# Performance work log

Measured on AMD Instinct MI355X. Metric: run time of the kernel, lower is better.

Reference implementation:

```python
import jax, jax.numpy as jnp
import numpy as np

DT = 0.1
N_STEPS = 20
STEP_SIZE = DT / N_STEPS


def setup_inputs() -> dict:
    key = jax.random.key(0)
    ks = jax.random.split(key, 8)
    sizes = [1024, 2048, 2048, 10]
    batch = 4096
    inp = {
        "x": jax.random.uniform(ks[0], (batch, sizes[0]), dtype=jnp.float32),
        "w0": jax.random.normal(ks[1], (sizes[0], sizes[1]), dtype=jnp.float32) / np.sqrt(sizes[0]),
        "w1": jax.random.normal(ks[2], (sizes[1], sizes[2]), dtype=jnp.float32) / np.sqrt(sizes[1]),
        "w2": jax.random.normal(ks[3], (sizes[2], sizes[3]), dtype=jnp.float32) / np.sqrt(sizes[2]),
        "b0": jnp.zeros((sizes[1],), jnp.float32),
        "b1": jnp.zeros((sizes[2],), jnp.float32),
        "b2": jnp.zeros((sizes[3],), jnp.float32),
        "s1": jax.random.uniform(ks[4], (batch, sizes[1]), dtype=jnp.float32),
        "s2": jax.random.uniform(ks[5], (batch, sizes[2]), dtype=jnp.float32),
        "s3": jax.random.uniform(ks[6], (batch, sizes[3]), dtype=jnp.float32),
    }
    return inp


def reference(x, w0, w1, w2, b0, b1, b2, s1, s2, s3):
    weights = [w0, w1, w2]
    biases = [b0, b1, b2]
    sig = jax.nn.sigmoid

    def dsig(v):
        s = sig(v)
        return s * (1.0 - s)

    def body(states, _):
        st = list(states)  # [s0(=x, clamped), s1, s2, s3]
        # hidden layers (indices 1..len-2), sequential in-place semantics
        for i in range(1, 3):
            pre = sig(st[i - 1]) @ weights[i - 1] + sig(st[i + 1]) @ weights[i].T + biases[i - 1]
            grad = dsig(st[i]) * pre - st[i]
            st[i] = st[i] - STEP_SIZE * grad
        # output layer (no target / beta=0 in eval mode)
        grad = dsig(st[3]) * (sig(st[2]) @ weights[2] + biases[2]) - st[3]
        st[3] = st[3] - STEP_SIZE * grad
        return tuple(st), None

    init = (x, s1, s2, s3)
    final, _ = jax.lax.scan(body, init, None, length=N_STEPS)
    return final[-1]
```

## Files before the change

kernel.cpp:

```cpp
#include <hip/hip_runtime.h>
#include <cstdint>
#include <cstddef>

using u16 = unsigned short;
using u32 = unsigned int;

typedef __bf16 bf16x8 __attribute__((ext_vector_type(8)));
typedef float f32x4 __attribute__((ext_vector_type(4)));
typedef u16 u16x4 __attribute__((ext_vector_type(4)));

#define DEV __device__ __forceinline__

constexpr float SS = 0.1f / 20.0f;

DEV float sigm(float x) { return 1.0f / (1.0f + __expf(-x)); }

DEV u16 f2bf(float f) {
  union { float f; u32 u; } v; v.f = f;
  u32 r = v.u + 0x7FFFu + ((v.u >> 16) & 1u);
  return (u16)(r >> 16);
}
DEV float bf2f(u16 h) {
  union { u32 u; float f; } v; v.u = ((u32)h) << 16;
  return v.f;
}

__global__ void k_prep(const float* __restrict__ in, float* __restrict__ fcopy,
                       float* __restrict__ sigf32, u16* __restrict__ sigb,
                       u16* __restrict__ rawb, int n) {
  int stride = gridDim.x * blockDim.x;
  for (int i = blockIdx.x * blockDim.x + threadIdx.x; i < n; i += stride) {
    float v = in[i];
    if (fcopy) fcopy[i] = v;
    if (rawb) rawb[i] = f2bf(v);
    if (sigf32 || sigb) {
      float s = sigm(v);
      if (sigf32) sigf32[i] = s;
      if (sigb) sigb[i] = f2bf(s);
    }
  }
}

__global__ void k_transpose_bf16(const float* __restrict__ in, u16* __restrict__ out,
                                 int K, int N) {
  __shared__ float tile[32][33];
  int kb = blockIdx.x * 32, nb = blockIdx.y * 32;
  int tx = threadIdx.x & 31, ty = threadIdx.x >> 5;
#pragma unroll
  for (int i = 0; i < 4; ++i)
    tile[ty + 8 * i][tx] = in[(size_t)(kb + ty + 8 * i) * N + nb + tx];
  __syncthreads();
#pragma unroll
  for (int i = 0; i < 4; ++i)
    out[(size_t)(nb + ty + 8 * i) * K + kb + tx] = f2bf(tile[tx][ty + 8 * i]);
}

DEV void tile_base(int b, int& tm, int& tn) {
  int xcd = b & 7, slot = b >> 3;
  tm = ((((xcd >> 1) << 3) | (slot >> 3))) * 128;
  tn = ((((xcd & 1) << 3) | (slot & 7))) * 128;
}

__global__ void k_init_state(const float* __restrict__ src, float* __restrict__ dst_swz) {
  int b = blockIdx.x;
  int tm, tn; tile_base(b, tm, tn);
  int tid = threadIdx.x, lane = tid & 63, wid = tid >> 6;
  int l15 = lane & 15, lhi = lane >> 4;
  int wm = (wid >> 2) * 64, wn = (wid & 3) * 32;
#pragma unroll
  for (int i = 0; i < 4; ++i)
#pragma unroll
    for (int j = 0; j < 2; ++j) {
      int gr = tm + wm + i * 16 + l15;
      int gc0 = tn + wn + j * 16 + 4 * lhi;
      f32x4 v = *(const f32x4*)(src + (size_t)gr * 2048 + gc0);
      *(f32x4*)(dst_swz + (((size_t)b * 8 + i * 2 + j) * 512 + tid) * 4) = v;
    }
}

template <int MODE>
__launch_bounds__(512, 4)
__global__ void k_gemm(const u16* __restrict__ A, const u16* __restrict__ Bt,
                       int M, int N, int K,
                       const u16* __restrict__ addcb, const float* __restrict__ bias,
                       const float* __restrict__ sig3, const float* __restrict__ w2,
                       float* __restrict__ statef, u16* __restrict__ sigb) {
  constexpr int BM = 128, BN = 128, BK = 64;
  __shared__ __align__(16) u16 Als[2][BM * BK];
  __shared__ __align__(16) u16 Bls[2][BN * BK];
  int b = blockIdx.x;
  int tm, tn; tile_base(b, tm, tn);
  int tid = threadIdx.x;
  int lane = tid & 63, wid = tid >> 6;
  int l15 = lane & 15, lhi = lane >> 4;
  int wm = (wid >> 2) * 64, wn = (wid & 3) * 32;

  const u16* Ag = A + (size_t)tm * K;
  const u16* Bg = Bt + (size_t)tn * K;

  f32x4 acc[4][2] = {};

  auto stage = [&](int buf, int k0) {
#pragma unroll
    for (int rd = 0; rd < 2; ++rd) {
      int S = rd * 512 + tid;
      int row = S >> 3;
      int cs = ((S & 7) ^ (row & 7)) * 8;
      __builtin_amdgcn_global_load_lds(
          (const __attribute__((address_space(1))) u32*)(Ag + (size_t)row * K + k0 + cs),
          (__attribute__((address_space(3))) u32*)(&Als[buf][0] + S * 8), 16, 0, 0);
      __builtin_amdgcn_global_load_lds(
          (const __attribute__((address_space(1))) u32*)(Bg + (size_t)row * K + k0 + cs),
          (__attribute__((address_space(3))) u32*)(&Bls[buf][0] + S * 8), 16, 0, 0);
    }
  };

  auto compute = [&](int buf) {
    __builtin_amdgcn_s_setprio(1);
#pragma unroll
    for (int s = 0; s < 2; ++s) {
      bf16x8 af[4], bfr[2];
#pragma unroll
      for (int i = 0; i < 4; ++i) {
        int row = wm + i * 16 + l15;
        af[i] = *(const bf16x8*)(&Als[buf][0] + row * BK + (((s * 4 + lhi) ^ (row & 7)) * 8));
      }
#pragma unroll
      for (int j = 0; j < 2; ++j) {
        int row = wn + j * 16 + l15;
        bfr[j] = *(const bf16x8*)(&Bls[buf][0] + row * BK + (((s * 4 + lhi) ^ (row & 7)) * 8));
      }
#pragma unroll
      for (int i = 0; i < 4; ++i)
#pragma unroll
        for (int j = 0; j < 2; ++j)
          acc[i][j] = __builtin_amdgcn_mfma_f32_16x16x32_bf16(bfr[j], af[i], acc[i][j], 0, 0, 0);
    }
    __builtin_amdgcn_s_setprio(0);
  };

  const int nt = K / BK;
  stage(0, 0);
  stage(1, BK);
  asm volatile("s_waitcnt vmcnt(4)" ::: "memory");
  __builtin_amdgcn_s_barrier();
  asm volatile("" ::: "memory");

  int t = 0;
  for (; t + 3 < nt; t += 2) {
    compute(0);
    asm volatile("" ::: "memory");
    __builtin_amdgcn_s_barrier();
    asm volatile("" ::: "memory");
    stage(0, (t + 2) * BK);
    asm volatile("s_waitcnt vmcnt(4)" ::: "memory");
    __builtin_amdgcn_s_barrier();
    asm volatile("" ::: "memory");

    compute(1);
    asm volatile("" ::: "memory");
    __builtin_amdgcn_s_barrier();
    asm volatile("" ::: "memory");
    stage(1, (t + 3) * BK);
    asm volatile("s_waitcnt vmcnt(4)" ::: "memory");
    __builtin_amdgcn_s_barrier();
    asm volatile("" ::: "memory");
  }
  compute(0);
  asm volatile("s_waitcnt vmcnt(0)" ::: "memory");
  __builtin_amdgcn_s_barrier();
  asm volatile("" ::: "memory");
  compute(1);

  if constexpr (MODE == 0) {
#pragma unroll
    for (int i = 0; i < 4; ++i)
#pragma unroll
      for (int j = 0; j < 2; ++j) {
        int gc0 = tn + wn + j * 16 + 4 * lhi;
        size_t sidx = (((size_t)b * 8 + i * 2 + j) * 512 + tid) * 4;
        u16x4 sb;
#pragma unroll
        for (int rr = 0; rr < 4; ++rr) sb[rr] = f2bf(acc[i][j][rr] + bias[gc0 + rr]);
        *(u16x4*)(sigb + sidx) = sb;
      }
  } else if constexpr (MODE == 1) {
#pragma unroll
    for (int i = 0; i < 4; ++i)
#pragma unroll
      for (int j = 0; j < 2; ++j) {
        int gr = tm + wm + i * 16 + l15;
        int gc0 = tn + wn + j * 16 + 4 * lhi;
        size_t sidx = (((size_t)b * 8 + i * 2 + j) * 512 + tid) * 4;
        u16x4 ab = *(const u16x4*)(addcb + sidx);
        f32x4 old = *(const f32x4*)(statef + sidx);
        f32x4 nv; u16x4 sb;
#pragma unroll
        for (int rr = 0; rr < 4; ++rr) {
          float pre = acc[i][j][rr] + bf2f(ab[rr]);
          float o = old[rr];
          float sg = sigm(o);
          float n = o - SS * (sg * (1.0f - sg) * pre - o);
          nv[rr] = n; sb[rr] = f2bf(sigm(n));
        }
        *(f32x4*)(statef + sidx) = nv;
        *(u16x4*)(sigb + (size_t)gr * N + gc0) = sb;
      }
  } else {
    float s3v[4][10];
#pragma unroll
    for (int i = 0; i < 4; ++i) {
      int gr = tm + wm + i * 16 + l15;
#pragma unroll
      for (int k = 0; k < 10; ++k) s3v[i][k] = sig3[gr * 10 + k];
    }
#pragma unroll
    for (int j = 0; j < 2; ++j) {
      int gc0 = tn + wn + j * 16 + 4 * lhi;
      float wv[4][10]; f32x4 bb;
#pragma unroll
      for (int rr = 0; rr < 4; ++rr) {
        bb[rr] = bias[gc0 + rr];
#pragma unroll
        for (int k = 0; k < 10; ++k) wv[rr][k] = w2[(gc0 + rr) * 10 + k];
      }
#pragma unroll
      for (int i = 0; i < 4; ++i) {
        int gr = tm + wm + i * 16 + l15;
        size_t sidx = (((size_t)b * 8 + i * 2 + j) * 512 + tid) * 4;
        f32x4 old = *(const f32x4*)(statef + sidx);
        f32x4 nv; u16x4 sb;
#pragma unroll
        for (int rr = 0; rr < 4; ++rr) {
          float ex = bb[rr];
#pragma unroll
          for (int k = 0; k < 10; ++k) ex += s3v[i][k] * wv[rr][k];
          float pre = acc[i][j][rr] + ex;
          float o = old[rr];
          float sg = sigm(o);
          float n = o - SS * (sg * (1.0f - sg) * pre - o);
          nv[rr] = n; sb[rr] = f2bf(sigm(n));
        }
        *(f32x4*)(statef + sidx) = nv;
        *(u16x4*)(sigb + (size_t)gr * N + gc0) = sb;
      }
    }
  }
}

__global__ void k_out(const u16* __restrict__ sigs2b, const float* __restrict__ w2,
                      const float* __restrict__ b2, float* __restrict__ s3f,
                      float* __restrict__ sigs3f, float* __restrict__ outOrNull) {
  int tid = threadIdx.x;
  int r = tid >> 4, l16 = tid & 15;
  int row = blockIdx.x * 16 + r;
  float acc[10] = {};
  const u16* arow = sigs2b + (size_t)row * 2048;
  for (int kb = l16; kb < 256; kb += 16) {
    u16x4 v0 = *(const u16x4*)(arow + kb * 8);
    u16x4 v1 = *(const u16x4*)(arow + kb * 8 + 4);
    float a[8];
#pragma unroll
    for (int e = 0; e < 4; ++e) { a[e] = bf2f(v0[e]); a[e + 4] = bf2f(v1[e]); }
    const float* wr = w2 + (size_t)kb * 80;
#pragma unroll
    for (int e = 0; e < 8; ++e)
#pragma unroll
      for (int n = 0; n < 10; ++n) acc[n] += a[e] * wr[e * 10 + n];
  }
#pragma unroll
  for (int m = 1; m < 16; m <<= 1)
#pragma unroll
    for (int n = 0; n < 10; ++n) acc[n] += __shfl_xor(acc[n], m, 64);
  if (l16 < 10) {
    float pre = 0.0f;
#pragma unroll
    for (int n = 0; n < 10; ++n)
      if (l16 == n) pre = acc[n];
    pre += b2[l16];
    size_t idx = (size_t)row * 10 + l16;
    float old = s3f[idx];
    float sg = sigm(old);
    float nv = old - SS * (sg * (1.0f - sg) * pre - old);
    s3f[idx] = nv;
    sigs3f[idx] = sigm(nv);
    if (outOrNull) outOrNull[idx] = nv;
  }
}

extern "C" void kernel_launch(void* const* d_in, const int* in_sizes, int n_in,
                              void* d_out, int out_size, void* d_ws, size_t ws_size,
                              hipStream_t stream) {
  const float* x  = (const float*)d_in[0];
  const float* w0 = (const float*)d_in[1];
  const float* w1 = (const float*)d_in[2];
  const float* w2 = (const float*)d_in[3];
  const float* b0 = (const float*)d_in[4];
  const float* b1 = (const float*)d_in[5];
  const float* b2 = (const float*)d_in[6];
  const float* s1 = (const float*)d_in[7];
  const float* s2 = (const float*)d_in[8];
  const float* s3 = (const float*)d_in[9];
  float* out = (float*)d_out;

  uint8_t* p = (uint8_t*)d_ws;
  auto alloc = [&](size_t bytes) {
    uint8_t* r = p;
    p += (bytes + 255) & ~(size_t)255;
    return r;
  };
  float* s1f    = (float*)alloc(4096ull * 2048 * 4);
  float* s2f    = (float*)alloc(4096ull * 2048 * 4);
  u16*   addcb  = (u16*)alloc(4096ull * 2048 * 2);
  u16*   sigs1b = (u16*)alloc(4096ull * 2048 * 2);
  u16*   sigs2b = (u16*)alloc(4096ull * 2048 * 2);
  u16*   sigxb  = (u16*)alloc(4096ull * 1024 * 2);
  u16*   w1b    = (u16*)alloc(2048ull * 2048 * 2);
  u16*   w1tb   = (u16*)alloc(2048ull * 2048 * 2);
  u16*   w0tb   = (u16*)alloc(2048ull * 1024 * 2);
  float* s3f    = (float*)alloc(4096ull * 10 * 4);
  float* sigs3f = (float*)alloc(4096ull * 10 * 4);
  (void)ws_size; (void)in_sizes; (void)n_in; (void)out_size;

  auto grid = [](int n) { int g = (n + 255) / 256; return g > 2048 ? 2048 : g; };

  k_prep<<<grid(4096 * 1024), 256, 0, stream>>>(x, nullptr, nullptr, sigxb, nullptr, 4096 * 1024);
  k_prep<<<grid(2048 * 2048), 256, 0, stream>>>(w1, nullptr, nullptr, nullptr, w1b, 2048 * 2048);
  k_prep<<<grid(4096 * 2048), 256, 0, stream>>>(s2, nullptr, nullptr, sigs2b, nullptr, 4096 * 2048);
  k_prep<<<grid(40960), 256, 0, stream>>>(s3, s3f, sigs3f, nullptr, nullptr, 40960);
  k_init_state<<<512, 512, 0, stream>>>(s1, s1f);
  k_init_state<<<512, 512, 0, stream>>>(s2, s2f);
  k_transpose_bf16<<<dim3(1024 / 32, 2048 / 32), 256, 0, stream>>>(w0, w0tb, 1024, 2048);
  k_transpose_bf16<<<dim3(2048 / 32, 2048 / 32), 256, 0, stream>>>(w1, w1tb, 2048, 2048);

  k_gemm<0><<<512, 512, 0, stream>>>(sigxb, w0tb, 4096, 2048, 1024,
                                     nullptr, b0, nullptr, nullptr, nullptr, addcb);

  for (int t = 0; t < 20; ++t) {
    k_gemm<1><<<512, 512, 0, stream>>>(sigs2b, w1b, 4096, 2048, 2048,
                                       addcb, nullptr, nullptr, nullptr, s1f, sigs1b);
    k_gemm<2><<<512, 512, 0, stream>>>(sigs1b, w1tb, 4096, 2048, 2048,
                                       nullptr, b1, sigs3f, w2, s2f, sigs2b);
    k_out<<<256, 256, 0, stream>>>(sigs2b, w2, b2, s3f, sigs3f, (t == 19) ? out : nullptr);
  }
}
```

Measured before the change: 2.503 ms.

## Enlarge GEMM tiles to 256x128 with triple-buffered LDS pipeline

Doubles the GEMM block tile height to 256 rows and gives each wave a 64x64 sub-tile, halving the grid to 256 blocks. Shared memory moves to dynamic allocation with three stages instead of two, and the k-loop becomes a rotating single-step prefetch. This aims to raise MFMA work per LDS and global load and to hide memory latency better. The trade-off is one block per CU with more registers per thread and a large LDS footprint.

```diff
diff --git a/kernel.cpp b/kernel.cpp
--- a/kernel.cpp
+++ b/kernel.cpp
@@ -57,8 +57,8 @@
 
 DEV void tile_base(int b, int& tm, int& tn) {
   int xcd = b & 7, slot = b >> 3;
-  tm = ((((xcd >> 1) << 3) | (slot >> 3))) * 128;
-  tn = ((((xcd & 1) << 3) | (slot & 7))) * 128;
+  tm = ((xcd >> 1) * 4 + (slot >> 3)) * 256;
+  tn = ((xcd & 1) * 8 + (slot & 7)) * 128;
 }
 
 __global__ void k_init_state(const float* __restrict__ src, float* __restrict__ dst_swz) {
@@ -66,119 +66,125 @@
   int tm, tn; tile_base(b, tm, tn);
   int tid = threadIdx.x, lane = tid & 63, wid = tid >> 6;
   int l15 = lane & 15, lhi = lane >> 4;
-  int wm = (wid >> 2) * 64, wn = (wid & 3) * 32;
+  int wm = (wid >> 1) * 64, wn = (wid & 1) * 64;
 #pragma unroll
   for (int i = 0; i < 4; ++i)
 #pragma unroll
-    for (int j = 0; j < 2; ++j) {
+    for (int j = 0; j < 4; ++j) {
       int gr = tm + wm + i * 16 + l15;
       int gc0 = tn + wn + j * 16 + 4 * lhi;
       f32x4 v = *(const f32x4*)(src + (size_t)gr * 2048 + gc0);
-      *(f32x4*)(dst_swz + (((size_t)b * 8 + i * 2 + j) * 512 + tid) * 4) = v;
+      *(f32x4*)(dst_swz + (((size_t)b * 16 + i * 4 + j) * 512 + tid) * 4) = v;
     }
 }
 
 template <int MODE>
-__launch_bounds__(512, 4)
+__launch_bounds__(512, 2)
 __global__ void k_gemm(const u16* __restrict__ A, const u16* __restrict__ Bt,
                        int M, int N, int K,
                        const u16* __restrict__ addcb, const float* __restrict__ bias,
                        const float* __restrict__ sig3, const float* __restrict__ w2,
                        float* __restrict__ statef, u16* __restrict__ sigb) {
-  constexpr int BM = 128, BN = 128, BK = 64;
-  __shared__ __align__(16) u16 Als[2][BM * BK];
-  __shared__ __align__(16) u16 Bls[2][BN * BK];
+  constexpr int BK = 64;
+  extern __shared__ __align__(16) u16 lds_dyn[];
+  u16* const AlsBase = lds_dyn;
+  u16* const BlsBase = lds_dyn + 3 * 16384;
+
   int b = blockIdx.x;
   int tm, tn; tile_base(b, tm, tn);
   int tid = threadIdx.x;
   int lane = tid & 63, wid = tid >> 6;
   int l15 = lane & 15, lhi = lane >> 4;
-  int wm = (wid >> 2) * 64, wn = (wid & 3) * 32;
+  int wm = (wid >> 1) * 64, wn = (wid & 1) * 64;
 
   const u16* Ag = A + (size_t)tm * K;
   const u16* Bg = Bt + (size_t)tn * K;
 
-  f32x4 acc[4][2] = {};
-
-  auto stage = [&](int buf, int k0) {
+  f32x4 acc[4][4] = {};
+
+  auto stage = [&](int p, int k0) {
+    u16* Ap = AlsBase + p * 16384;
+    u16* Bp = BlsBase + p * 8192;
+#pragma unroll
+    for (int rd = 0; rd < 4; ++rd) {
+      int S = rd * 512 + tid;
+      int row = S >> 3;
+      int cs = ((S & 7) ^ (row & 7)) * 8;
+      __builtin_amdgcn_global_load_lds(
+          (const __attribute__((address_space(1))) u32*)(Ag + (size_t)row * K + k0 + cs),
+          (__attribute__((address_space(3))) u32*)(Ap + S * 8), 16, 0, 0);
+    }
 #pragma unroll
     for (int rd = 0; rd < 2; ++rd) {
       int S = rd * 512 + tid;
       int row = S >> 3;
       int cs = ((S & 7) ^ (row & 7)) * 8;
       __builtin_amdgcn_global_load_lds(
-          (const __attribute__((address_space(1))) u32*)(Ag + (size_t)row * K + k0 + cs),
-          (__attribute__((address_space(3))) u32*)(&Als[buf][0] + S * 8), 16, 0, 0);
-      __builtin_amdgcn_global_load_lds(
           (const __attribute__((address_space(1))) u32*)(Bg + (size_t)row * K + k0 + cs),
-          (__attribute__((address_space(3))) u32*)(&Bls[buf][0] + S * 8), 16, 0, 0);
+          (__attribute__((address_space(3))) u32*)(Bp + S * 8), 16, 0, 0);
     }
   };
 
-  auto compute = [&](int buf) {
+  auto compute = [&](int p) {
+    const u16* Ap = AlsBase + p * 16384;
+    const u16* Bp = BlsBase + p * 8192;
     __builtin_amdgcn_s_setprio(1);
 #pragma unroll
     for (int s = 0; s < 2; ++s) {
-      bf16x8 af[4], bfr[2];
+      bf16x8 af[4], bfr[4];
 #pragma unroll
       for (int i = 0; i < 4; ++i) {
         int row = wm + i * 16 + l15;
-        af[i] = *(const bf16x8*)(&Als[buf][0] + row * BK + (((s * 4 + lhi) ^ (row & 7)) * 8));
-      }
-#pragma unroll
-      for (int j = 0; j < 2; ++j) {
+        af[i] = *(const bf16x8*)(Ap + row * BK + (((s * 4 + lhi) ^ (row & 7)) * 8));
+      }
+#pragma unroll
+      for (int j = 0; j < 4; ++j) {
         int row = wn + j * 16 + l15;
-        bfr[j] = *(const bf16x8*)(&Bls[buf][0] + row * BK + (((s * 4 + lhi) ^ (row & 7)) * 8));
+        bfr[j] = *(const bf16x8*)(Bp + row * BK + (((s * 4 + lhi) ^ (row & 7)) * 8));
       }
 #pragma unroll
       for (int i = 0; i < 4; ++i)
 #pragma unroll
-        for (int j = 0; j < 2; ++j)
+        for (int j = 0; j < 4; ++j)
           acc[i][j] = __builtin_amdgcn_mfma_f32_16x16x32_bf16(bfr[j], af[i], acc[i][j], 0, 0, 0);
     }
     __builtin_amdgcn_s_setprio(0);
   };
 
   const int nt = K / BK;
-  stage(0, 0);
-  stage(1, BK);
-  asm volatile("s_waitcnt vmcnt(4)" ::: "memory");
-  __builtin_amdgcn_s_barrier();
-  asm volatile("" ::: "memory");
-
-  int t = 0;
-  for (; t + 3 < nt; t += 2) {
-    compute(0);
+  stage(0, 0); stage(1, BK); stage(2, 2 * BK);
+  int p = 0;
+  for (int t = 0; t < nt - 3; ++t) {
+    asm volatile("s_waitcnt vmcnt(12)" ::: "memory");
+    __builtin_amdgcn_s_barrier();
+    asm volatile("" ::: "memory");
+    compute(p);
     asm volatile("" ::: "memory");
     __builtin_amdgcn_s_barrier();
     asm volatile("" ::: "memory");
-    stage(0, (t + 2) * BK);
-    asm volatile("s_waitcnt vmcnt(4)" ::: "memory");
-    __builtin_amdgcn_s_barrier();
-    asm volatile("" ::: "memory");
-
-    compute(1);
-    asm volatile("" ::: "memory");
-    __builtin_amdgcn_s_barrier();
-    asm volatile("" ::: "memory");
-    stage(1, (t + 3) * BK);
-    asm volatile("s_waitcnt vmcnt(4)" ::: "memory");
-    __builtin_amdgcn_s_barrier();
-    asm volatile("" ::: "memory");
-  }
-  compute(0);
+    stage(p, (t + 3) * BK);
+    p = (p == 2) ? 0 : p + 1;
+  }
+  asm volatile("s_waitcnt vmcnt(12)" ::: "memory");
+  __builtin_amdgcn_s_barrier();
+  asm volatile("" ::: "memory");
+  compute(p); p = (p == 2) ? 0 : p + 1;
+  asm volatile("s_waitcnt vmcnt(6)" ::: "memory");
+  __builtin_amdgcn_s_barrier();
+  asm volatile("" ::: "memory");
+  compute(p); p = (p == 2) ? 0 : p + 1;
   asm volatile("s_waitcnt vmcnt(0)" ::: "memory");
   __builtin_amdgcn_s_barrier();
   asm volatile("" ::: "memory");
-  compute(1);
+  compute(p);
 
   if constexpr (MODE == 0) {
 #pragma unroll
     for (int i = 0; i < 4; ++i)
 #pragma unroll
-      for (int j = 0; j < 2; ++j) {
+      for (int j = 0; j < 4; ++j) {
         int gc0 = tn + wn + j * 16 + 4 * lhi;
-        size_t sidx = (((size_t)b * 8 + i * 2 + j) * 512 + tid) * 4;
+        size_t sidx = (((size_t)b * 16 + i * 4 + j) * 512 + tid) * 4;
         u16x4 sb;
 #pragma unroll
         for (int rr = 0; rr < 4; ++rr) sb[rr] = f2bf(acc[i][j][rr] + bias[gc0 + rr]);
@@ -188,10 +194,10 @@
 #pragma unroll
     for (int i = 0; i < 4; ++i)
 #pragma unroll
-      for (int j = 0; j < 2; ++j) {
+      for (int j = 0; j < 4; ++j) {
         int gr = tm + wm + i * 16 + l15;
         int gc0 = tn + wn + j * 16 + 4 * lhi;
-        size_t sidx = (((size_t)b * 8 + i * 2 + j) * 512 + tid) * 4;
+        size_t sidx = (((size_t)b * 16 + i * 4 + j) * 512 + tid) * 4;
         u16x4 ab = *(const u16x4*)(addcb + sidx);
         f32x4 old = *(const f32x4*)(statef + sidx);
         f32x4 nv; u16x4 sb;
@@ -215,7 +221,7 @@
       for (int k = 0; k < 10; ++k) s3v[i][k] = sig3[gr * 10 + k];
     }
 #pragma unroll
-    for (int j = 0; j < 2; ++j) {
+    for (int j = 0; j < 4; ++j) {
       int gc0 = tn + wn + j * 16 + 4 * lhi;
       float wv[4][10]; f32x4 bb;
 #pragma unroll
@@ -227,7 +233,7 @@
 #pragma unroll
       for (int i = 0; i < 4; ++i) {
         int gr = tm + wm + i * 16 + l15;
-        size_t sidx = (((size_t)b * 8 + i * 2 + j) * 512 + tid) * 4;
+        size_t sidx = (((size_t)b * 16 + i * 4 + j) * 512 + tid) * 4;
         f32x4 old = *(const f32x4*)(statef + sidx);
         f32x4 nv; u16x4 sb;
 #pragma unroll
@@ -322,25 +328,33 @@
   float* sigs3f = (float*)alloc(4096ull * 10 * 4);
   (void)ws_size; (void)in_sizes; (void)n_in; (void)out_size;
 
+  constexpr int LDS_BYTES = 3 * (16384 + 8192) * 2;
+  (void)hipFuncSetAttribute((const void*)k_gemm<0>,
+      hipFuncAttributeMaxDynamicSharedMemorySize, LDS_BYTES);
+  (void)hipFuncSetAttribute((const void*)k_gemm<1>,
+      hipFuncAttributeMaxDynamicSharedMemorySize, LDS_BYTES);
+  (void)hipFuncSetAttribute((const void*)k_gemm<2>,
+      hipFuncAttributeMaxDynamicSharedMemorySize, LDS_BYTES);
+
   auto grid = [](int n) { int g = (n + 255) / 256; return g > 2048 ? 2048 : g; };
 
   k_prep<<<grid(4096 * 1024), 256, 0, stream>>>(x, nullptr, nullptr, sigxb, nullptr, 4096 * 1024);
   k_prep<<<grid(2048 * 2048), 256, 0, stream>>>(w1, nullptr, nullptr, nullptr, w1b, 2048 * 2048);
   k_prep<<<grid(4096 * 2048), 256, 0, stream>>>(s2, nullptr, nullptr, sigs2b, nullptr, 4096 * 2048);
   k_prep<<<grid(40960), 256, 0, stream>>>(s3, s3f, sigs3f, nullptr, nullptr, 40960);
-  k_init_state<<<512, 512, 0, stream>>>(s1, s1f);
-  k_init_state<<<512, 512, 0, stream>>>(s2, s2f);
+  k_init_state<<<256, 512, 0, stream>>>(s1, s1f);
+  k_init_state<<<256, 512, 0, stream>>>(s2, s2f);
   k_transpose_bf16<<<dim3(1024 / 32, 2048 / 32), 256, 0, stream>>>(w0, w0tb, 1024, 2048);
   k_transpose_bf16<<<dim3(2048 / 32, 2048 / 32), 256, 0, stream>>>(w1, w1tb, 2048, 2048);
 
-  k_gemm<0><<<512, 512, 0, stream>>>(sigxb, w0tb, 4096, 2048, 1024,
-                                     nullptr, b0, nullptr, nullptr, nullptr, addcb);
+  k_gemm<0><<<256, 512, LDS_BYTES, stream>>>(sigxb, w0tb, 4096, 2048, 1024,
+                                             nullptr, b0, nullptr, nullptr, nullptr, addcb);
 
   for (int t = 0; t < 20; ++t) {
-    k_gemm<1><<<512, 512, 0, stream>>>(sigs2b, w1b, 4096, 2048, 2048,
-                                       addcb, nullptr, nullptr, nullptr, s1f, sigs1b);
-    k_gemm<2><<<512, 512, 0, stream>>>(sigs1b, w1tb, 4096, 2048, 2048,
-                                       nullptr, b1, sigs3f, w2, s2f, sigs2b);
+    k_gemm<1><<<256, 512, LDS_BYTES, stream>>>(sigs2b, w1b, 4096, 2048, 2048,
+                                               addcb, nullptr, nullptr, nullptr, s1f, sigs1b);
+    k_gemm<2><<<256, 512, LDS_BYTES, stream>>>(sigs1b, w1tb, 4096, 2048, 2048,
+                                               nullptr, b1, sigs3f, w2, s2f, sigs2b);
     k_out<<<256, 256, 0, stream>>>(sigs2b, w2, b2, s3f, sigs3f, (t == 19) ? out : nullptr);
   }
 }
```

New measurement: 2.493 ms. About the same (-0.4%).

## Switch GEMM mainloop to 4-stage BK=32 LDS pipeline with deeper prefetch

Applied to the files above, without the earlier changes.

The GEMM mainloop moves from a double-buffered BK=64 scheme to a four-buffer ring with BK=32 and three K-slices in flight. Each thread issues one global-to-LDS load per operand per stage, and the XOR swizzle is adjusted to 4 chunks per row. The aim is to hide global memory latency better by keeping more loads outstanding. In exchange, each K-step does half as many MFMAs between two barriers, so synchronisation overhead per FLOP doubles, and swizzling over 4 chunks may cause more LDS bank conflicts.

```diff
diff --git a/kernel.cpp b/kernel.cpp
--- a/kernel.cpp
+++ b/kernel.cpp
@@ -85,9 +85,10 @@
                        const u16* __restrict__ addcb, const float* __restrict__ bias,
                        const float* __restrict__ sig3, const float* __restrict__ w2,
                        float* __restrict__ statef, u16* __restrict__ sigb) {
-  constexpr int BM = 128, BN = 128, BK = 64;
-  __shared__ __align__(16) u16 Als[2][BM * BK];
-  __shared__ __align__(16) u16 Bls[2][BN * BK];
+  constexpr int BK = 32;
+  constexpr int BUFE = 128 * BK;
+  __shared__ __align__(16) u16 Als[4][BUFE];
+  __shared__ __align__(16) u16 Bls[4][BUFE];
   int b = blockIdx.x;
   int tm, tn; tile_base(b, tm, tn);
   int tid = threadIdx.x;
@@ -100,77 +101,62 @@
 
   f32x4 acc[4][2] = {};
 
-  auto stage = [&](int buf, int k0) {
-#pragma unroll
-    for (int rd = 0; rd < 2; ++rd) {
-      int S = rd * 512 + tid;
-      int row = S >> 3;
-      int cs = ((S & 7) ^ (row & 7)) * 8;
-      __builtin_amdgcn_global_load_lds(
-          (const __attribute__((address_space(1))) u32*)(Ag + (size_t)row * K + k0 + cs),
-          (__attribute__((address_space(3))) u32*)(&Als[buf][0] + S * 8), 16, 0, 0);
-      __builtin_amdgcn_global_load_lds(
-          (const __attribute__((address_space(1))) u32*)(Bg + (size_t)row * K + k0 + cs),
-          (__attribute__((address_space(3))) u32*)(&Bls[buf][0] + S * 8), 16, 0, 0);
-    }
+  int srow = tid >> 2;
+  int scs = (((tid & 3) ^ (srow & 3)) * 8);
+  auto stage = [&](int p, int k0) {
+    __builtin_amdgcn_global_load_lds(
+        (const __attribute__((address_space(1))) u32*)(Ag + (size_t)srow * K + k0 + scs),
+        (__attribute__((address_space(3))) u32*)(&Als[p][0] + tid * 8), 16, 0, 0);
+    __builtin_amdgcn_global_load_lds(
+        (const __attribute__((address_space(1))) u32*)(Bg + (size_t)srow * K + k0 + scs),
+        (__attribute__((address_space(3))) u32*)(&Bls[p][0] + tid * 8), 16, 0, 0);
   };
 
-  auto compute = [&](int buf) {
+  auto compute = [&](int p) {
     __builtin_amdgcn_s_setprio(1);
-#pragma unroll
-    for (int s = 0; s < 2; ++s) {
-      bf16x8 af[4], bfr[2];
-#pragma unroll
-      for (int i = 0; i < 4; ++i) {
-        int row = wm + i * 16 + l15;
-        af[i] = *(const bf16x8*)(&Als[buf][0] + row * BK + (((s * 4 + lhi) ^ (row & 7)) * 8));
-      }
-#pragma unroll
-      for (int j = 0; j < 2; ++j) {
-        int row = wn + j * 16 + l15;
-        bfr[j] = *(const bf16x8*)(&Bls[buf][0] + row * BK + (((s * 4 + lhi) ^ (row & 7)) * 8));
-      }
-#pragma unroll
-      for (int i = 0; i < 4; ++i)
-#pragma unroll
-        for (int j = 0; j < 2; ++j)
-          acc[i][j] = __builtin_amdgcn_mfma_f32_16x16x32_bf16(bfr[j], af[i], acc[i][j], 0, 0, 0);
-    }
+    bf16x8 af[4], bfr[2];
+#pragma unroll
+    for (int i = 0; i < 4; ++i) {
+      int row = wm + i * 16 + l15;
+      af[i] = *(const bf16x8*)(&Als[p][0] + row * BK + ((lhi ^ (row & 3)) * 8));
+    }
+#pragma unroll
+    for (int j = 0; j < 2; ++j) {
+      int row = wn + j * 16 + l15;
+      bfr[j] = *(const bf16x8*)(&Bls[p][0] + row * BK + ((lhi ^ (row & 3)) * 8));
+    }
+#pragma unroll
+    for (int i = 0; i < 4; ++i)
+#pragma unroll
+      for (int j = 0; j < 2; ++j)
+        acc[i][j] = __builtin_amdgcn_mfma_f32_16x16x32_bf16(bfr[j], af[i], acc[i][j], 0, 0, 0);
     __builtin_amdgcn_s_setprio(0);
   };
 
   const int nt = K / BK;
-  stage(0, 0);
-  stage(1, BK);
+  stage(0, 0); stage(1, BK); stage(2, 2 * BK);
+  for (int t = 0; t < nt - 3; ++t) {
+    stage((t + 3) & 3, (t + 3) * BK);
+    asm volatile("s_waitcnt vmcnt(6)" ::: "memory");
+    __builtin_amdgcn_s_barrier();
+    asm volatile("" ::: "memory");
+    compute(t & 3);
+    asm volatile("" ::: "memory");
+    __builtin_amdgcn_s_barrier();
+    asm volatile("" ::: "memory");
+  }
   asm volatile("s_waitcnt vmcnt(4)" ::: "memory");
   __builtin_amdgcn_s_barrier();
   asm volatile("" ::: "memory");
-
-  int t = 0;
-  for (; t + 3 < nt; t += 2) {
-    compute(0);
-    asm volatile("" ::: "memory");
-    __builtin_amdgcn_s_barrier();
-    asm volatile("" ::: "memory");
-    stage(0, (t + 2) * BK);
-    asm volatile("s_waitcnt vmcnt(4)" ::: "memory");
-    __builtin_amdgcn_s_barrier();
-    asm volatile("" ::: "memory");
-
-    compute(1);
-    asm volatile("" ::: "memory");
-    __builtin_amdgcn_s_barrier();
-    asm volatile("" ::: "memory");
-    stage(1, (t + 3) * BK);
-    asm volatile("s_waitcnt vmcnt(4)" ::: "memory");
-    __builtin_amdgcn_s_barrier();
-    asm volatile("" ::: "memory");
-  }
-  compute(0);
+  compute((nt - 3) & 3);
+  asm volatile("s_waitcnt vmcnt(2)" ::: "memory");
+  __builtin_amdgcn_s_barrier();
+  asm volatile("" ::: "memory");
+  compute((nt - 2) & 3);
   asm volatile("s_waitcnt vmcnt(0)" ::: "memory");
   __builtin_amdgcn_s_barrier();
   asm volatile("" ::: "memory");
-  compute(1);
+  compute((nt - 1) & 3);
 
   if constexpr (MODE == 0) {
 #pragma unroll
```

Result: slower. 2.906 ms (+16.1%).

## Switch GEMM operands from bf16 to scaled fp8 with LDS-staged epilogue stores

Applied to the files above, without the earlier changes.

All GEMM operands (sigmoid activations and weights scaled by 32) are quantized to fp8 and multiplied with fp8 MFMA, with a K-tile of 128 bytes per stage. The aim is to halve operand bytes and use the higher fp8 matrix throughput. The epilogues now stage the fp8 sigmoid output through LDS so it can be written in coalesced 16-byte rows. This also changes the MODE 2 epilogue to reload sig3 and w2 per element, and it risks accuracy loss from fp8 e4m3 quantization.

```diff
diff --git a/kernel.cpp b/kernel.cpp
--- a/kernel.cpp
+++ b/kernel.cpp
@@ -2,16 +2,20 @@
 #include <cstdint>
 #include <cstddef>
 
+using u8  = unsigned char;
 using u16 = unsigned short;
 using u32 = unsigned int;
 
-typedef __bf16 bf16x8 __attribute__((ext_vector_type(8)));
 typedef float f32x4 __attribute__((ext_vector_type(4)));
 typedef u16 u16x4 __attribute__((ext_vector_type(4)));
+typedef u32 u32x2 __attribute__((ext_vector_type(2)));
+typedef u32 u32x4 __attribute__((ext_vector_type(4)));
 
 #define DEV __device__ __forceinline__
 
 constexpr float SS = 0.1f / 20.0f;
+constexpr float WSC = 32.0f;
+constexpr float WINV = 1.0f / 32.0f;
 
 DEV float sigm(float x) { return 1.0f / (1.0f + __expf(-x)); }
 
@@ -24,25 +28,36 @@
   union { u32 u; float f; } v; v.u = ((u32)h) << 16;
   return v.f;
 }
+DEV u32 pk4_fp8(float a, float b, float c, float d) {
+  u32 r = (u32)__builtin_amdgcn_cvt_pk_fp8_f32(a, b, 0, false);
+  r = (u32)__builtin_amdgcn_cvt_pk_fp8_f32(c, d, (int)r, true);
+  return r;
+}
 
 __global__ void k_prep(const float* __restrict__ in, float* __restrict__ fcopy,
-                       float* __restrict__ sigf32, u16* __restrict__ sigb,
-                       u16* __restrict__ rawb, int n) {
+                       float* __restrict__ sigf32, int n) {
   int stride = gridDim.x * blockDim.x;
   for (int i = blockIdx.x * blockDim.x + threadIdx.x; i < n; i += stride) {
     float v = in[i];
     if (fcopy) fcopy[i] = v;
-    if (rawb) rawb[i] = f2bf(v);
-    if (sigf32 || sigb) {
-      float s = sigm(v);
-      if (sigf32) sigf32[i] = s;
-      if (sigb) sigb[i] = f2bf(s);
-    }
-  }
-}
-
-__global__ void k_transpose_bf16(const float* __restrict__ in, u16* __restrict__ out,
-                                 int K, int N) {
+    if (sigf32) sigf32[i] = sigm(v);
+  }
+}
+
+__global__ void k_prep8(const float* __restrict__ in, u8* __restrict__ out,
+                        int n4, int dosig, float scale) {
+  int stride = gridDim.x * blockDim.x;
+  for (int i = blockIdx.x * blockDim.x + threadIdx.x; i < n4; i += stride) {
+    f32x4 v = *(const f32x4*)(in + (size_t)i * 4);
+    float a, b, c, d;
+    if (dosig) { a = sigm(v[0]); b = sigm(v[1]); c = sigm(v[2]); d = sigm(v[3]); }
+    else       { a = v[0] * scale; b = v[1] * scale; c = v[2] * scale; d = v[3] * scale; }
+    *(u32*)(out + (size_t)i * 4) = pk4_fp8(a, b, c, d);
+  }
+}
+
+__global__ void k_transpose_fp8(const float* __restrict__ in, u8* __restrict__ out,
+                                int K, int N, float scale) {
   __shared__ float tile[32][33];
   int kb = blockIdx.x * 32, nb = blockIdx.y * 32;
   int tx = threadIdx.x & 31, ty = threadIdx.x >> 5;
@@ -50,9 +65,17 @@
   for (int i = 0; i < 4; ++i)
     tile[ty + 8 * i][tx] = in[(size_t)(kb + ty + 8 * i) * N + nb + tx];
   __syncthreads();
-#pragma unroll
-  for (int i = 0; i < 4; ++i)
-    out[(size_t)(nb + ty + 8 * i) * K + kb + tx] = f2bf(tile[tx][ty + 8 * i]);
+  if (tx < 8) {
+#pragma unroll
+    for (int i = 0; i < 4; ++i) {
+      int orow = nb + ty + 8 * i;
+      u32 r = pk4_fp8(tile[tx * 4 + 0][ty + 8 * i] * scale,
+                      tile[tx * 4 + 1][ty + 8 * i] * scale,
+                      tile[tx * 4 + 2][ty + 8 * i] * scale,
+                      tile[tx * 4 + 3][ty + 8 * i] * scale);
+      *(u32*)(out + (size_t)orow * K + kb + tx * 4) = r;
+    }
+  }
 }
 
 DEV void tile_base(int b, int& tm, int& tn) {
@@ -80,14 +103,18 @@
 
 template <int MODE>
 __launch_bounds__(512, 4)
-__global__ void k_gemm(const u16* __restrict__ A, const u16* __restrict__ Bt,
-                       int M, int N, int K,
+__global__ void k_gemm(const u8* __restrict__ A, const u8* __restrict__ Bt,
+                       int N, int K,
                        const u16* __restrict__ addcb, const float* __restrict__ bias,
                        const float* __restrict__ sig3, const float* __restrict__ w2,
-                       float* __restrict__ statef, u16* __restrict__ sigb) {
-  constexpr int BM = 128, BN = 128, BK = 64;
-  __shared__ __align__(16) u16 Als[2][BM * BK];
-  __shared__ __align__(16) u16 Bls[2][BN * BK];
+                       float* __restrict__ statef, u16* __restrict__ sigb16,
+                       u8* __restrict__ sig8) {
+  __shared__ __align__(16) u8 lds8[65536];
+  u8* const Als0 = lds8;
+  u8* const Als1 = lds8 + 16384;
+  u8* const Bls0 = lds8 + 32768;
+  u8* const Bls1 = lds8 + 49152;
+
   int b = blockIdx.x;
   int tm, tn; tile_base(b, tm, tn);
   int tid = threadIdx.x;
@@ -95,53 +122,62 @@
   int l15 = lane & 15, lhi = lane >> 4;
   int wm = (wid >> 2) * 64, wn = (wid & 3) * 32;
 
-  const u16* Ag = A + (size_t)tm * K;
-  const u16* Bg = Bt + (size_t)tn * K;
+  const u8* Ag = A + (size_t)tm * K;
+  const u8* Bg = Bt + (size_t)tn * K;
 
   f32x4 acc[4][2] = {};
 
-  auto stage = [&](int buf, int k0) {
+  auto stage = [&](int buf, int t) {
+    u8* Ap = buf ? Als1 : Als0;
+    u8* Bp = buf ? Bls1 : Bls0;
+    int k0 = t * 128;
 #pragma unroll
     for (int rd = 0; rd < 2; ++rd) {
       int S = rd * 512 + tid;
       int row = S >> 3;
-      int cs = ((S & 7) ^ (row & 7)) * 8;
+      int cs = ((S & 7) ^ (row & 7)) * 16;
       __builtin_amdgcn_global_load_lds(
           (const __attribute__((address_space(1))) u32*)(Ag + (size_t)row * K + k0 + cs),
-          (__attribute__((address_space(3))) u32*)(&Als[buf][0] + S * 8), 16, 0, 0);
+          (__attribute__((address_space(3))) u32*)(Ap + S * 16), 16, 0, 0);
       __builtin_amdgcn_global_load_lds(
           (const __attribute__((address_space(1))) u32*)(Bg + (size_t)row * K + k0 + cs),
-          (__attribute__((address_space(3))) u32*)(&Bls[buf][0] + S * 8), 16, 0, 0);
+          (__attribute__((address_space(3))) u32*)(Bp + S * 16), 16, 0, 0);
     }
   };
 
   auto compute = [&](int buf) {
+    const u8* Ap = buf ? Als1 : Als0;
+    const u8* Bp = buf ? Bls1 : Bls0;
+    int sub = (lhi & 1) * 8;
     __builtin_amdgcn_s_setprio(1);
 #pragma unroll
-    for (int s = 0; s < 2; ++s) {
-      bf16x8 af[4], bfr[2];
+    for (int s = 0; s < 4; ++s) {
+      int so = s * 2 + (lhi >> 1);
+      u32x2 af[4], bfr[2];
 #pragma unroll
       for (int i = 0; i < 4; ++i) {
         int row = wm + i * 16 + l15;
-        af[i] = *(const bf16x8*)(&Als[buf][0] + row * BK + (((s * 4 + lhi) ^ (row & 7)) * 8));
+        af[i] = *(const u32x2*)(Ap + row * 128 + ((so ^ (row & 7)) * 16) + sub);
       }
 #pragma unroll
       for (int j = 0; j < 2; ++j) {
         int row = wn + j * 16 + l15;
-        bfr[j] = *(const bf16x8*)(&Bls[buf][0] + row * BK + (((s * 4 + lhi) ^ (row & 7)) * 8));
+        bfr[j] = *(const u32x2*)(Bp + row * 128 + ((so ^ (row & 7)) * 16) + sub);
       }
 #pragma unroll
       for (int i = 0; i < 4; ++i)
 #pragma unroll
         for (int j = 0; j < 2; ++j)
-          acc[i][j] = __builtin_amdgcn_mfma_f32_16x16x32_bf16(bfr[j], af[i], acc[i][j], 0, 0, 0);
+          acc[i][j] = __builtin_amdgcn_mfma_f32_16x16x32_fp8_fp8(
+              __builtin_bit_cast(long, bfr[j]), __builtin_bit_cast(long, af[i]),
+              acc[i][j], 0, 0, 0);
     }
     __builtin_amdgcn_s_setprio(0);
   };
 
-  const int nt = K / BK;
+  const int nt = K / 128;
   stage(0, 0);
-  stage(1, BK);
+  stage(1, 1);
   asm volatile("s_waitcnt vmcnt(4)" ::: "memory");
   __builtin_amdgcn_s_barrier();
   asm volatile("" ::: "memory");
@@ -152,7 +188,7 @@
     asm volatile("" ::: "memory");
     __builtin_amdgcn_s_barrier();
     asm volatile("" ::: "memory");
-    stage(0, (t + 2) * BK);
+    stage(0, t + 2);
     asm volatile("s_waitcnt vmcnt(4)" ::: "memory");
     __builtin_amdgcn_s_barrier();
     asm volatile("" ::: "memory");
@@ -161,7 +197,7 @@
     asm volatile("" ::: "memory");
     __builtin_amdgcn_s_barrier();
     asm volatile("" ::: "memory");
-    stage(1, (t + 3) * BK);
+    stage(1, t + 3);
     asm volatile("s_waitcnt vmcnt(4)" ::: "memory");
     __builtin_amdgcn_s_barrier();
     asm volatile("" ::: "memory");
@@ -181,92 +217,80 @@
         size_t sidx = (((size_t)b * 8 + i * 2 + j) * 512 + tid) * 4;
         u16x4 sb;
 #pragma unroll
-        for (int rr = 0; rr < 4; ++rr) sb[rr] = f2bf(acc[i][j][rr] + bias[gc0 + rr]);
-        *(u16x4*)(sigb + sidx) = sb;
+        for (int rr = 0; rr < 4; ++rr)
+          sb[rr] = f2bf(acc[i][j][rr] * WINV + bias[gc0 + rr]);
+        *(u16x4*)(sigb16 + sidx) = sb;
       }
-  } else if constexpr (MODE == 1) {
+  } else {
+    asm volatile("" ::: "memory");
+    __builtin_amdgcn_s_barrier();
+    asm volatile("" ::: "memory");
+    u8* T = lds8;
 #pragma unroll
     for (int i = 0; i < 4; ++i)
 #pragma unroll
       for (int j = 0; j < 2; ++j) {
-        int gr = tm + wm + i * 16 + l15;
-        int gc0 = tn + wn + j * 16 + 4 * lhi;
         size_t sidx = (((size_t)b * 8 + i * 2 + j) * 512 + tid) * 4;
-        u16x4 ab = *(const u16x4*)(addcb + sidx);
         f32x4 old = *(const f32x4*)(statef + sidx);
-        f32x4 nv; u16x4 sb;
+        f32x4 nv; float sv[4];
 #pragma unroll
         for (int rr = 0; rr < 4; ++rr) {
-          float pre = acc[i][j][rr] + bf2f(ab[rr]);
+          float pre = acc[i][j][rr] * WINV;
+          if constexpr (MODE == 1) {
+            u16x4 ab = *(const u16x4*)(addcb + sidx);
+            pre += bf2f(ab[rr]);
+          } else {
+            int gc = tn + wn + j * 16 + 4 * lhi + rr;
+            float ex = bias[gc];
+            int gr = tm + wm + i * 16 + l15;
+#pragma unroll
+            for (int k = 0; k < 10; ++k) ex += sig3[gr * 10 + k] * w2[gc * 10 + k];
+            pre += ex;
+          }
           float o = old[rr];
           float sg = sigm(o);
           float n = o - SS * (sg * (1.0f - sg) * pre - o);
-          nv[rr] = n; sb[rr] = f2bf(sigm(n));
+          nv[rr] = n; sv[rr] = sigm(n);
         }
         *(f32x4*)(statef + sidx) = nv;
-        *(u16x4*)(sigb + (size_t)gr * N + gc0) = sb;
+        int grl = wm + i * 16 + l15;
+        int gcl = wn + j * 16 + 4 * lhi;
+        *(u32*)(T + grl * 144 + gcl) = pk4_fp8(sv[0], sv[1], sv[2], sv[3]);
       }
-  } else {
-    float s3v[4][10];
-#pragma unroll
-    for (int i = 0; i < 4; ++i) {
-      int gr = tm + wm + i * 16 + l15;
-#pragma unroll
-      for (int k = 0; k < 10; ++k) s3v[i][k] = sig3[gr * 10 + k];
-    }
-#pragma unroll
-    for (int j = 0; j < 2; ++j) {
-      int gc0 = tn + wn + j * 16 + 4 * lhi;
-      float wv[4][10]; f32x4 bb;
-#pragma unroll
-      for (int rr = 0; rr < 4; ++rr) {
-        bb[rr] = bias[gc0 + rr];
-#pragma unroll
-        for (int k = 0; k < 10; ++k) wv[rr][k] = w2[(gc0 + rr) * 10 + k];
-      }
-#pragma unroll
-      for (int i = 0; i < 4; ++i) {
-        int gr = tm + wm + i * 16 + l15;
-        size_t sidx = (((size_t)b * 8 + i * 2 + j) * 512 + tid) * 4;
-        f32x4 old = *(const f32x4*)(statef + sidx);
-        f32x4 nv; u16x4 sb;
-#pragma unroll
-        for (int rr = 0; rr < 4; ++rr) {
-          float ex = bb[rr];
-#pragma unroll
-          for (int k = 0; k < 10; ++k) ex += s3v[i][k] * wv[rr][k];
-          float pre = acc[i][j][rr] + ex;
-          float o = old[rr];
-          float sg = sigm(o);
-          float n = o - SS * (sg * (1.0f - sg) * pre - o);
-          nv[rr] = n; sb[rr] = f2bf(sigm(n));
-        }
-        *(f32x4*)(statef + sidx) = nv;
-        *(u16x4*)(sigb + (size_t)gr * N + gc0) = sb;
-      }
-    }
-  }
-}
-
-__global__ void k_out(const u16* __restrict__ sigs2b, const float* __restrict__ w2,
+    asm volatile("s_waitcnt lgkmcnt(0)" ::: "memory");
+    __builtin_amdgcn_s_barrier();
+    asm volatile("" ::: "memory");
+#pragma unroll
+    for (int rd = 0; rd < 2; ++rd) {
+      int S = rd * 512 + tid;
+      int r = S >> 3, c = S & 7;
+      u32x4 v = *(const u32x4*)(T + r * 144 + c * 16);
+      *(u32x4*)(sig8 + (size_t)(tm + r) * N + tn + c * 16) = v;
+    }
+  }
+}
+
+__global__ void k_out(const u8* __restrict__ sigs2b8, const float* __restrict__ w2,
                       const float* __restrict__ b2, float* __restrict__ s3f,
                       float* __restrict__ sigs3f, float* __restrict__ outOrNull) {
   int tid = threadIdx.x;
   int r = tid >> 4, l16 = tid & 15;
   int row = blockIdx.x * 16 + r;
   float acc[10] = {};
-  const u16* arow = sigs2b + (size_t)row * 2048;
-  for (int kb = l16; kb < 256; kb += 16) {
-    u16x4 v0 = *(const u16x4*)(arow + kb * 8);
-    u16x4 v1 = *(const u16x4*)(arow + kb * 8 + 4);
-    float a[8];
-#pragma unroll
-    for (int e = 0; e < 4; ++e) { a[e] = bf2f(v0[e]); a[e + 4] = bf2f(v1[e]); }
-    const float* wr = w2 + (size_t)kb * 80;
-#pragma unroll
-    for (int e = 0; e < 8; ++e)
-#pragma unroll
-      for (int n = 0; n < 10; ++n) acc[n] += a[e] * wr[e * 10 + n];
+  const u32x4* arow = (const u32x4*)(sigs2b8 + (size_t)row * 2048);
+  for (int kb = l16; kb < 128; kb += 16) {
+    u32x4 v = arow[kb];
+#pragma unroll
+    for (int w = 0; w < 4; ++w) {
+      const float* wr = w2 + (size_t)(kb * 16 + w * 4) * 10;
+      float f0 = __builtin_amdgcn_cvt_f32_fp8((int)v[w], 0);
+      float f1 = __builtin_amdgcn_cvt_f32_fp8((int)v[w], 1);
+      float f2 = __builtin_amdgcn_cvt_f32_fp8((int)v[w], 2);
+      float f3 = __builtin_amdgcn_cvt_f32_fp8((int)v[w], 3);
+#pragma unroll
+      for (int n = 0; n < 10; ++n)
+        acc[n] += f0 * wr[n] + f1 * wr[10 + n] + f2 * wr[20 + n] + f3 * wr[30 + n];
+    }
   }
 #pragma unroll
   for (int m = 1; m < 16; m <<= 1)
@@ -312,35 +336,38 @@
   float* s1f    = (float*)alloc(4096ull * 2048 * 4);
   float* s2f    = (float*)alloc(4096ull * 2048 * 4);
   u16*   addcb  = (u16*)alloc(4096ull * 2048 * 2);
-  u16*   sigs1b = (u16*)alloc(4096ull * 2048 * 2);
-  u16*   sigs2b = (u16*)alloc(4096ull * 2048 * 2);
-  u16*   sigxb  = (u16*)alloc(4096ull * 1024 * 2);
-  u16*   w1b    = (u16*)alloc(2048ull * 2048 * 2);
-  u16*   w1tb   = (u16*)alloc(2048ull * 2048 * 2);
-  u16*   w0tb   = (u16*)alloc(2048ull * 1024 * 2);
+  u8*    sigs1b = (u8*)alloc(4096ull * 2048);
+  u8*    sigs2b = (u8*)alloc(4096ull * 2048);
+  u8*    sigxb  = (u8*)alloc(4096ull * 1024);
+  u8*    w1b    = (u8*)alloc(2048ull * 2048);
+  u8*    w1tb   = (u8*)alloc(2048ull * 2048);
+  u8*    w0tb   = (u8*)alloc(2048ull * 1024);
   float* s3f    = (float*)alloc(4096ull * 10 * 4);
   float* sigs3f = (float*)alloc(4096ull * 10 * 4);
   (void)ws_size; (void)in_sizes; (void)n_in; (void)out_size;
 
   auto grid = [](int n) { int g = (n + 255) / 256; return g > 2048 ? 2048 : g; };
 
-  k_prep<<<grid(4096 * 1024), 256, 0, stream>>>(x, nullptr, nullptr, sigxb, nullptr, 4096 * 1024);
-  k_prep<<<grid(2048 * 2048), 256, 0, stream>>>(w1, nullptr, nullptr, nullptr, w1b, 2048 * 2048);
-  k_prep<<<grid(4096 * 2048), 256, 0, stream>>>(s2, nullptr, nullptr, sigs2b, nullptr, 4096 * 2048);
-  k_prep<<<grid(40960), 256, 0, stream>>>(s3, s3f, sigs3f, nullptr, nullptr, 40960);
+  k_prep8<<<grid(4096 * 1024 / 4), 256, 0, stream>>>(x, sigxb, 4096 * 1024 / 4, 1, 1.0f);
+  k_prep8<<<grid(2048 * 2048 / 4), 256, 0, stream>>>(w1, w1b, 2048 * 2048 / 4, 0, WSC);
+  k_prep8<<<grid(4096 * 2048 / 4), 256, 0, stream>>>(s2, sigs2b, 4096 * 2048 / 4, 1, 1.0f);
+  k_prep<<<grid(40960), 256, 0, stream>>>(s3, s3f, sigs3f, 40960);
   k_init_state<<<512, 512, 0, stream>>>(s1, s1f);
   k_init_state<<<512, 512, 0, stream>>>(s2, s2f);
-  k_transpose_bf16<<<dim3(1024 / 32, 2048 / 32), 256, 0, stream>>>(w0, w0tb, 1024, 2048);
-  k_transpose_bf16<<<dim3(2048 / 32, 2048 / 32), 256, 0, stream>>>(w1, w1tb, 2048, 2048);
-
-  k_gemm<0><<<512, 512, 0, stream>>>(sigxb, w0tb, 4096, 2048, 1024,
-                                     nullptr, b0, nullptr, nullptr, nullptr, addcb);
+  k_transpose_fp8<<<dim3(1024 / 32, 2048 / 32), 256, 0, stream>>>(w0, w0tb, 1024, 2048, WSC);
+  k_transpose_fp8<<<dim3(2048 / 32, 2048 / 32), 256, 0, stream>>>(w1, w1tb, 2048, 2048, WSC);
+
+  k_gemm<0><<<512, 512, 0, stream>>>(sigxb, w0tb, 2048, 1024,
+                                     nullptr, b0, nullptr, nullptr,
+                                     nullptr, addcb, nullptr);
 
   for (int t = 0; t < 20; ++t) {
-    k_gemm<1><<<512, 512, 0, stream>>>(sigs2b, w1b, 4096, 2048, 2048,
-                                       addcb, nullptr, nullptr, nullptr, s1f, sigs1b);
-    k_gemm<2><<<512, 512, 0, stream>>>(sigs1b, w1tb, 4096, 2048, 2048,
-                                       nullptr, b1, sigs3f, w2, s2f, sigs2b);
+    k_gemm<1><<<512, 512, 0, stream>>>(sigs2b, w1b, 2048, 2048,
+                                       addcb, nullptr, nullptr, nullptr,
+                                       s1f, nullptr, sigs1b);
+    k_gemm<2><<<512, 512, 0, stream>>>(sigs1b, w1tb, 2048, 2048,
+                                       nullptr, b1, sigs3f, w2,
+                                       s2f, nullptr, sigs2b);
     k_out<<<256, 256, 0, stream>>>(sigs2b, w2, b2, s3f, sigs3f, (t == 19) ? out : nullptr);
   }
 }
```

Result: slower. 4.059 ms (+62.2%).
